# Kernel tuning notes

Measured on AMD Instinct MI355X. Metric: run time of the kernel, lower is better.

Reference implementation:

```python
import jax, jax.numpy as jnp
import numpy as np

# Grid config (from VoxelGrid.from_config defaults / args_to_config)
LOWER = jnp.array([-4.0, -4.0, -1.0], dtype=jnp.float32)
UPPER = jnp.array([4.0, 4.0, 1.0], dtype=jnp.float32)
RESOLUTION = 25.0
SIZE = (200, 200, 50)  # ceil((upper - lower) * resolution)
N_POINTS = 8388608


def setup_inputs() -> dict:
    key = jax.random.key(0)
    k1, k2 = jax.random.split(key)
    # query points uniform over (slightly beyond) the grid extent; points whose
    # fractional index falls outside [0, size-1] are masked to 0 as in the module
    u = jax.random.uniform(k1, (N_POINTS, 3), dtype=jnp.float32)
    x = LOWER + u * (UPPER - LOWER)
    # learned parameter hk.get_parameter('grid', (*size, 1)); randn instead of
    # zeros-init so outputs/grads are nontrivial
    grid = jax.random.normal(k2, (*SIZE, 1), dtype=jnp.float32) * 0.1
    return {"x": x, "grid": grid}


def _trilinear(x, grid):
    size_i = jnp.array(SIZE, dtype=jnp.int32)
    size_f = jnp.array(SIZE, dtype=jnp.float32)
    idx = (x - LOWER) * RESOLUTION                       # [N, 3] fractional index
    valid = jnp.all((idx >= 0.0) & (idx <= size_f - 1.0), axis=-1)  # [N]
    i0 = jnp.clip(jnp.floor(idx).astype(jnp.int32), 0, size_i - 1)  # [N, 3]
    i1 = jnp.minimum(i0 + 1, size_i - 1)                 # [N, 3]
    f = idx - jnp.floor(idx)                             # [N, 3] trilinear fractions
    w = jnp.stack([1.0 - f, f], axis=-1)                 # [N, 3, 2] per-axis weights
    corners = [(i0[:, d], i1[:, d]) for d in range(3)]
    acc = jnp.zeros(x.shape[0], dtype=grid.dtype)
    # 8 fixed corner gathers (structural, not a data-dim loop)
    for a in (0, 1):
        for b in (0, 1):
            for c in (0, 1):
                v = grid[corners[0][a], corners[1][b], corners[2][c], 0]  # [N]
                acc = acc + v * (w[:, 0, a] * w[:, 1, b] * w[:, 2, c])
    sigma = jnp.where(valid, acc, 0.0)
    return sigma


def reference(x, grid):
    sigma = _trilinear(x, grid)
    alpha = jnp.zeros_like(sigma)  # do_alpha=False -> alpha is constant 0
    return (sigma, alpha)
```

## Files before the change

kernel.cpp:

```cpp
#include <hip/hip_runtime.h>
#include <hip/hip_fp16.h>


constexpr int SX = 200, SY = 200, SZ = 50;
constexpr int NVOX = SX * SY * SZ;
constexpr int CX = SX - 1, CY = SY - 1, CZ = SZ - 1;
constexpr int NCELL = CX * CY * CZ;
constexpr int PPT = 4;
constexpr int BLK = 256;
constexpr int PPB = BLK * PPT;


__global__ __launch_bounds__(256) void grid_absmax(
    const float4* __restrict__ g4, unsigned int* __restrict__ scale_u)
{
    int tid = blockIdx.x * 256 + threadIdx.x;
    int stride = gridDim.x * 256;
    unsigned int u = 0;
    for (int i = tid; i < NVOX / 4; i += stride) {
        float4 v = g4[i];
        u = max(u, __float_as_uint(v.x) & 0x7fffffffu);
        u = max(u, __float_as_uint(v.y) & 0x7fffffffu);
        u = max(u, __float_as_uint(v.z) & 0x7fffffffu);
        u = max(u, __float_as_uint(v.w) & 0x7fffffffu);
    }
    #pragma unroll
    for (int off = 32; off > 0; off >>= 1)
        u = max(u, (unsigned int)__shfl_xor((int)u, off, 64));
    __shared__ unsigned int wmax[4];
    int lane = threadIdx.x & 63, wid = threadIdx.x >> 6;
    if (lane == 0) wmax[wid] = u;
    __syncthreads();
    if (threadIdx.x == 0) {
        unsigned int m = max(max(wmax[0], wmax[1]), max(wmax[2], wmax[3]));
        atomicMax(scale_u, m);
    }
}

__global__ __launch_bounds__(256) void build_cells_i8(
    const float* __restrict__ grid, uint2* __restrict__ rec,
    const unsigned int* __restrict__ scale_u)
{
    int i = blockIdx.x * 256 + threadIdx.x;
    if (i >= NCELL) return;
    float absmax = __uint_as_float(*scale_u);
    float inv = (absmax > 0.0f) ? 127.0f / absmax : 0.0f;

    int cz = i % CZ;
    int tmp = i / CZ;
    int cy = tmp % CY;
    int cx = tmp / CY;

    const float* g00 = grid + (cx * SY + cy) * SZ + cz;
    const float* g01 = g00 + SZ;
    const float* g10 = g00 + SY * SZ;
    const float* g11 = g10 + SZ;

    float v[8] = { g00[0], g00[1], g01[0], g01[1],
                   g10[0], g10[1], g11[0], g11[1] };
    unsigned int lo = 0, hi = 0;
    #pragma unroll
    for (int k = 0; k < 4; ++k) {
        int q = (int)rintf(v[k] * inv);
        q = min(max(q, -127), 127);
        lo |= ((unsigned int)(q & 0xff)) << (8 * k);
    }
    #pragma unroll
    for (int k = 0; k < 4; ++k) {
        int q = (int)rintf(v[4 + k] * inv);
        q = min(max(q, -127), 127);
        hi |= ((unsigned int)(q & 0xff)) << (8 * k);
    }
    rec[i] = make_uint2(lo, hi);
}

__device__ __forceinline__ float sb(unsigned int w, int k)
{
    return (float)((int)(w << (24 - 8 * k)) >> 24);
}

__global__ __launch_bounds__(256) void voxel_trilinear_i8(
    const float* __restrict__ x,
    const uint2* __restrict__ rec,
    const unsigned int* __restrict__ scale_u,
    float* __restrict__ out,
    int n)
{
    __shared__ float xs[3 * PPB];
    int tid = threadIdx.x;
    long long base = (long long)blockIdx.x * PPB;
    float s = __uint_as_float(*scale_u) * (1.0f / 127.0f);

    if (base + PPB <= n) {
        const float4* xg = (const float4*)(x + base * 3);
        float4* xl = (float4*)xs;
        #pragma unroll
        for (int j = 0; j < 3; ++j)
            xl[tid + BLK * j] = xg[tid + BLK * j];
    } else {
        for (int j = tid; j < 3 * PPB; j += BLK) {
            long long g = base * 3 + j;
            xs[j] = (g < 3LL * n) ? x[g] : 0.0f;
        }
    }
    __syncthreads();

    int   cell[PPT];
    float ux[PPT], uy[PPT], uz[PPT];
    bool  valid[PPT];

    #pragma unroll
    for (int k = 0; k < PPT; ++k) {
        int p = tid + BLK * k;
        float ix = (xs[3 * p + 0] + 4.0f) * 25.0f;
        float iy = (xs[3 * p + 1] + 4.0f) * 25.0f;
        float iz = (xs[3 * p + 2] + 1.0f) * 25.0f;
        valid[k] = (ix >= 0.0f) & (ix <= (float)(SX - 1)) &
                   (iy >= 0.0f) & (iy <= (float)(SY - 1)) &
                   (iz >= 0.0f) & (iz <= (float)(SZ - 1));
        int cx = min(max((int)floorf(ix), 0), SX - 2);
        int cy = min(max((int)floorf(iy), 0), SY - 2);
        int cz = min(max((int)floorf(iz), 0), SZ - 2);
        ux[k] = ix - (float)cx;
        uy[k] = iy - (float)cy;
        uz[k] = iz - (float)cz;
        cell[k] = (cx * CY + cy) * CZ + cz;
    }

    uint2 pk[PPT];
    #pragma unroll
    for (int k = 0; k < PPT; ++k)
        pk[k] = rec[cell[k]];

    #pragma unroll
    for (int k = 0; k < PPT; ++k) {
        unsigned int lo = pk[k].x, hi = pk[k].y;
        float vz = 1.0f - uz[k], vy = 1.0f - uy[k], vx = 1.0f - ux[k];
        float c00 = sb(lo, 0) * vz + sb(lo, 1) * uz[k];
        float c01 = sb(lo, 2) * vz + sb(lo, 3) * uz[k];
        float c10 = sb(hi, 0) * vz + sb(hi, 1) * uz[k];
        float c11 = sb(hi, 2) * vz + sb(hi, 3) * uz[k];
        float c0 = c00 * vy + c01 * uy[k];
        float c1 = c10 * vy + c11 * uy[k];
        float acc = (c0 * vx + c1 * ux[k]) * s;

        long long i = base + tid + BLK * k;
        if (i < n) {
            out[i] = valid[k] ? acc : 0.0f;
            out[n + i] = 0.0f;
        }
    }
}

__global__ __launch_bounds__(256) void convert_grid_fp16(
    const float* __restrict__ grid, __half* __restrict__ t)
{
    int i = blockIdx.x * 256 + threadIdx.x;
    if (i < NVOX) t[i] = __float2half(grid[i]);
}

__device__ __forceinline__ float2 ldpair(const __half* __restrict__ t, int idx)
{
    __half2 h;
    __builtin_memcpy(&h, t + idx, sizeof(__half2));
    return __half22float2(h);
}

__global__ __launch_bounds__(256) void voxel_trilinear_pair(
    const float* __restrict__ x, const __half* __restrict__ t,
    float* __restrict__ out, int n)
{
    int i = blockIdx.x * 256 + threadIdx.x;
    if (i >= n) return;
    float ix = (x[3 * i + 0] + 4.0f) * 25.0f;
    float iy = (x[3 * i + 1] + 4.0f) * 25.0f;
    float iz = (x[3 * i + 2] + 1.0f) * 25.0f;
    bool valid = (ix >= 0.0f) & (ix <= (float)(SX - 1)) &
                 (iy >= 0.0f) & (iy <= (float)(SY - 1)) &
                 (iz >= 0.0f) & (iz <= (float)(SZ - 1));
    float fx = floorf(ix), fy = floorf(iy), fz = floorf(iz);
    int ax = min(max((int)fx, 0), SX - 1);
    int ay = min(max((int)fy, 0), SY - 1);
    int bx = min(ax + 1, SX - 1);
    int by = min(ay + 1, SY - 1);
    int zc = min(max((int)fz, 0), SZ - 2);
    float u = iz - (float)zc, su = 1.0f - u;
    float tx = ix - fx, ty = iy - fy;
    float sx = 1.0f - tx, sy = 1.0f - ty;
    int r00 = (ax * SY + ay) * SZ + zc;
    int r01 = (ax * SY + by) * SZ + zc;
    int r10 = (bx * SY + ay) * SZ + zc;
    int r11 = (bx * SY + by) * SZ + zc;
    float2 p00 = ldpair(t, r00), p01 = ldpair(t, r01);
    float2 p10 = ldpair(t, r10), p11 = ldpair(t, r11);
    float c00 = p00.x * su + p00.y * u;
    float c01 = p01.x * su + p01.y * u;
    float c10 = p10.x * su + p10.y * u;
    float c11 = p11.x * su + p11.y * u;
    float c0 = c00 * sy + c01 * ty;
    float c1 = c10 * sy + c11 * ty;
    out[i] = valid ? (c0 * sx + c1 * tx) : 0.0f;
    out[n + i] = 0.0f;
}

extern "C" void kernel_launch(void* const* d_in, const int* in_sizes, int n_in,
                              void* d_out, int out_size, void* d_ws, size_t ws_size,
                              hipStream_t stream) {
    const float* x = (const float*)d_in[0];
    const float* grid = (const float*)d_in[1];
    float* out = (float*)d_out;
    int n = in_sizes[0] / 3;

    size_t rec_bytes = (size_t)NCELL * sizeof(uint2);
    if (ws_size >= rec_bytes + 4) {
        uint2* rec = (uint2*)d_ws;
        unsigned int* scale_u = (unsigned int*)((char*)d_ws + rec_bytes);
        hipMemsetAsync(scale_u, 0, 4, stream);
        grid_absmax<<<512, 256, 0, stream>>>((const float4*)grid, scale_u);
        build_cells_i8<<<(NCELL + 255) / 256, 256, 0, stream>>>(grid, rec, scale_u);
        int blocks = (n + PPB - 1) / PPB;
        voxel_trilinear_i8<<<blocks, BLK, 0, stream>>>(x, rec, scale_u, out, n);
    } else if (ws_size >= (size_t)NVOX * sizeof(__half)) {
        __half* t = (__half*)d_ws;
        convert_grid_fp16<<<(NVOX + 255) / 256, 256, 0, stream>>>(grid, t);
        voxel_trilinear_pair<<<(n + 255) / 256, 256, 0, stream>>>(x, t, out, n);
    }
}
```

Baseline: 272.6 us.

## Replace int8 8-corner cell records with 2-byte z-pair table and nontemporal IO

Swaps the 8-byte per-cell int8 record (about 15.6 MB) for a 2-byte z-pair table (about 3.9 MB), so each point now does four 2-byte gathers instead of one 8-byte gather. The table is small enough to stay in cache, while the per-point gather count rises. The atomic absmax plus memset is replaced by per-block partial maxima that are reduced inside the build kernel. Input loads and output stores now use nontemporal hints to keep the streamed data from pushing the table out of cache.

```diff
diff --git a/kernel.cpp b/kernel.cpp
--- a/kernel.cpp
+++ b/kernel.cpp
@@ -1,18 +1,21 @@
 #include <hip/hip_runtime.h>
-#include <hip/hip_fp16.h>
-
+
+
+typedef float vfloat4 __attribute__((ext_vector_type(4)));
 
 constexpr int SX = 200, SY = 200, SZ = 50;
 constexpr int NVOX = SX * SY * SZ;
-constexpr int CX = SX - 1, CY = SY - 1, CZ = SZ - 1;
-constexpr int NCELL = CX * CY * CZ;
+constexpr int CZ = SZ - 1;
+constexpr int NXY = SX * SY;
+constexpr int NREC = NXY * CZ;
 constexpr int PPT = 4;
 constexpr int BLK = 256;
 constexpr int PPB = BLK * PPT;
-
-
-__global__ __launch_bounds__(256) void grid_absmax(
-    const float4* __restrict__ g4, unsigned int* __restrict__ scale_u)
+constexpr int NPART = 512;
+
+
+__global__ __launch_bounds__(256) void grid_absmax_part(
+    const float4* __restrict__ g4, unsigned int* __restrict__ part)
 {
     int tid = blockIdx.x * 256 + threadIdx.x;
     int stride = gridDim.x * 256;
@@ -31,72 +34,70 @@
     int lane = threadIdx.x & 63, wid = threadIdx.x >> 6;
     if (lane == 0) wmax[wid] = u;
     __syncthreads();
+    if (threadIdx.x == 0)
+        part[blockIdx.x] = max(max(wmax[0], wmax[1]), max(wmax[2], wmax[3]));
+}
+
+__global__ __launch_bounds__(256) void build_pairs_i8(
+    const float* __restrict__ grid, unsigned short* __restrict__ tp,
+    const unsigned int* __restrict__ part, float* __restrict__ scale_f)
+{
+    __shared__ unsigned int wmax[4];
+    __shared__ float s_inv;
+    unsigned int u = max(part[threadIdx.x], part[threadIdx.x + 256]);
+    #pragma unroll
+    for (int off = 32; off > 0; off >>= 1)
+        u = max(u, (unsigned int)__shfl_xor((int)u, off, 64));
+    int lane = threadIdx.x & 63, wid = threadIdx.x >> 6;
+    if (lane == 0) wmax[wid] = u;
+    __syncthreads();
     if (threadIdx.x == 0) {
         unsigned int m = max(max(wmax[0], wmax[1]), max(wmax[2], wmax[3]));
-        atomicMax(scale_u, m);
-    }
-}
-
-__global__ __launch_bounds__(256) void build_cells_i8(
-    const float* __restrict__ grid, uint2* __restrict__ rec,
-    const unsigned int* __restrict__ scale_u)
-{
+        float absmax = __uint_as_float(m);
+        s_inv = (absmax > 0.0f) ? 127.0f / absmax : 0.0f;
+        if (blockIdx.x == 0) *scale_f = absmax * (1.0f / 127.0f);
+    }
+    __syncthreads();
+    float inv = s_inv;
+
     int i = blockIdx.x * 256 + threadIdx.x;
-    if (i >= NCELL) return;
-    float absmax = __uint_as_float(*scale_u);
-    float inv = (absmax > 0.0f) ? 127.0f / absmax : 0.0f;
-
-    int cz = i % CZ;
-    int tmp = i / CZ;
-    int cy = tmp % CY;
-    int cx = tmp / CY;
-
-    const float* g00 = grid + (cx * SY + cy) * SZ + cz;
-    const float* g01 = g00 + SZ;
-    const float* g10 = g00 + SY * SZ;
-    const float* g11 = g10 + SZ;
-
-    float v[8] = { g00[0], g00[1], g01[0], g01[1],
-                   g10[0], g10[1], g11[0], g11[1] };
-    unsigned int lo = 0, hi = 0;
-    #pragma unroll
-    for (int k = 0; k < 4; ++k) {
-        int q = (int)rintf(v[k] * inv);
-        q = min(max(q, -127), 127);
-        lo |= ((unsigned int)(q & 0xff)) << (8 * k);
-    }
-    #pragma unroll
-    for (int k = 0; k < 4; ++k) {
-        int q = (int)rintf(v[4 + k] * inv);
-        q = min(max(q, -127), 127);
-        hi |= ((unsigned int)(q & 0xff)) << (8 * k);
-    }
-    rec[i] = make_uint2(lo, hi);
-}
-
-__device__ __forceinline__ float sb(unsigned int w, int k)
-{
-    return (float)((int)(w << (24 - 8 * k)) >> 24);
-}
-
-__global__ __launch_bounds__(256) void voxel_trilinear_i8(
+    if (i >= NREC) return;
+    int z = i % CZ;
+    int xy = i / CZ;
+    const float* g = grid + xy * SZ + z;
+    float a = g[0], b = g[1];
+    int qa = min(max((int)rintf(a * inv), -127), 127);
+    int qb = min(max((int)rintf(b * inv), -127), 127);
+    tp[i] = (unsigned short)((qa & 0xff) | ((qb & 0xff) << 8));
+}
+
+__device__ __forceinline__ float lob(unsigned int w)
+{
+    return (float)((int)(w << 24) >> 24);
+}
+__device__ __forceinline__ float hib(unsigned int w)
+{
+    return (float)((int)(w << 16) >> 24);
+}
+
+__global__ __launch_bounds__(256) void voxel_trilinear_zp(
     const float* __restrict__ x,
-    const uint2* __restrict__ rec,
-    const unsigned int* __restrict__ scale_u,
+    const unsigned short* __restrict__ tp,
+    const float* __restrict__ scale_f,
     float* __restrict__ out,
     int n)
 {
     __shared__ float xs[3 * PPB];
     int tid = threadIdx.x;
     long long base = (long long)blockIdx.x * PPB;
-    float s = __uint_as_float(*scale_u) * (1.0f / 127.0f);
+    float s = *scale_f;
 
     if (base + PPB <= n) {
-        const float4* xg = (const float4*)(x + base * 3);
-        float4* xl = (float4*)xs;
+        const vfloat4* xg = (const vfloat4*)(x + base * 3);
+        vfloat4* xl = (vfloat4*)xs;
         #pragma unroll
         for (int j = 0; j < 3; ++j)
-            xl[tid + BLK * j] = xg[tid + BLK * j];
+            xl[tid + BLK * j] = __builtin_nontemporal_load(&xg[tid + BLK * j]);
     } else {
         for (int j = tid; j < 3 * PPB; j += BLK) {
             long long g = base * 3 + j;
@@ -105,8 +106,8 @@
     }
     __syncthreads();
 
-    int   cell[PPT];
     float ux[PPT], uy[PPT], uz[PPT];
+    int   i00[PPT];
     bool  valid[PPT];
 
     #pragma unroll
@@ -124,50 +125,41 @@
         ux[k] = ix - (float)cx;
         uy[k] = iy - (float)cy;
         uz[k] = iz - (float)cz;
-        cell[k] = (cx * CY + cy) * CZ + cz;
-    }
-
-    uint2 pk[PPT];
-    #pragma unroll
-    for (int k = 0; k < PPT; ++k)
-        pk[k] = rec[cell[k]];
-
+        i00[k] = (cx * SY + cy) * CZ + cz;
+    }
+
+    unsigned int p00[PPT], p01[PPT], p10[PPT], p11[PPT];
     #pragma unroll
     for (int k = 0; k < PPT; ++k) {
-        unsigned int lo = pk[k].x, hi = pk[k].y;
-        float vz = 1.0f - uz[k], vy = 1.0f - uy[k], vx = 1.0f - ux[k];
-        float c00 = sb(lo, 0) * vz + sb(lo, 1) * uz[k];
-        float c01 = sb(lo, 2) * vz + sb(lo, 3) * uz[k];
-        float c10 = sb(hi, 0) * vz + sb(hi, 1) * uz[k];
-        float c11 = sb(hi, 2) * vz + sb(hi, 3) * uz[k];
+        int b = i00[k];
+        p00[k] = tp[b];
+        p01[k] = tp[b + CZ];
+        p10[k] = tp[b + SY * CZ];
+        p11[k] = tp[b + SY * CZ + CZ];
+    }
+
+    #pragma unroll
+    for (int k = 0; k < PPT; ++k) {
+        float w1 = uz[k], w0 = 1.0f - w1;
+        float c00 = lob(p00[k]) * w0 + hib(p00[k]) * w1;
+        float c01 = lob(p01[k]) * w0 + hib(p01[k]) * w1;
+        float c10 = lob(p10[k]) * w0 + hib(p10[k]) * w1;
+        float c11 = lob(p11[k]) * w0 + hib(p11[k]) * w1;
+        float vy = 1.0f - uy[k], vx = 1.0f - ux[k];
         float c0 = c00 * vy + c01 * uy[k];
         float c1 = c10 * vy + c11 * uy[k];
         float acc = (c0 * vx + c1 * ux[k]) * s;
 
         long long i = base + tid + BLK * k;
         if (i < n) {
-            out[i] = valid[k] ? acc : 0.0f;
-            out[n + i] = 0.0f;
+            __builtin_nontemporal_store(valid[k] ? acc : 0.0f, &out[i]);
+            __builtin_nontemporal_store(0.0f, &out[n + i]);
         }
     }
 }
 
-__global__ __launch_bounds__(256) void convert_grid_fp16(
-    const float* __restrict__ grid, __half* __restrict__ t)
-{
-    int i = blockIdx.x * 256 + threadIdx.x;
-    if (i < NVOX) t[i] = __float2half(grid[i]);
-}
-
-__device__ __forceinline__ float2 ldpair(const __half* __restrict__ t, int idx)
-{
-    __half2 h;
-    __builtin_memcpy(&h, t + idx, sizeof(__half2));
-    return __half22float2(h);
-}
-
-__global__ __launch_bounds__(256) void voxel_trilinear_pair(
-    const float* __restrict__ x, const __half* __restrict__ t,
+__global__ __launch_bounds__(256) void voxel_trilinear_direct(
+    const float* __restrict__ x, const float* __restrict__ grid,
     float* __restrict__ out, int n)
 {
     int i = blockIdx.x * 256 + threadIdx.x;
@@ -178,28 +170,23 @@
     bool valid = (ix >= 0.0f) & (ix <= (float)(SX - 1)) &
                  (iy >= 0.0f) & (iy <= (float)(SY - 1)) &
                  (iz >= 0.0f) & (iz <= (float)(SZ - 1));
-    float fx = floorf(ix), fy = floorf(iy), fz = floorf(iz);
-    int ax = min(max((int)fx, 0), SX - 1);
-    int ay = min(max((int)fy, 0), SY - 1);
-    int bx = min(ax + 1, SX - 1);
-    int by = min(ay + 1, SY - 1);
-    int zc = min(max((int)fz, 0), SZ - 2);
-    float u = iz - (float)zc, su = 1.0f - u;
-    float tx = ix - fx, ty = iy - fy;
-    float sx = 1.0f - tx, sy = 1.0f - ty;
-    int r00 = (ax * SY + ay) * SZ + zc;
-    int r01 = (ax * SY + by) * SZ + zc;
-    int r10 = (bx * SY + ay) * SZ + zc;
-    int r11 = (bx * SY + by) * SZ + zc;
-    float2 p00 = ldpair(t, r00), p01 = ldpair(t, r01);
-    float2 p10 = ldpair(t, r10), p11 = ldpair(t, r11);
-    float c00 = p00.x * su + p00.y * u;
-    float c01 = p01.x * su + p01.y * u;
-    float c10 = p10.x * su + p10.y * u;
-    float c11 = p11.x * su + p11.y * u;
-    float c0 = c00 * sy + c01 * ty;
-    float c1 = c10 * sy + c11 * ty;
-    out[i] = valid ? (c0 * sx + c1 * tx) : 0.0f;
+    int cx = min(max((int)floorf(ix), 0), SX - 2);
+    int cy = min(max((int)floorf(iy), 0), SY - 2);
+    int cz = min(max((int)floorf(iz), 0), SZ - 2);
+    float tx = ix - (float)cx, ty = iy - (float)cy, tz = iz - (float)cz;
+    const float* g = grid + (cx * SY + cy) * SZ + cz;
+    float v000 = g[0], v001 = g[1];
+    float v010 = g[SZ], v011 = g[SZ + 1];
+    float v100 = g[SY * SZ], v101 = g[SY * SZ + 1];
+    float v110 = g[SY * SZ + SZ], v111 = g[SY * SZ + SZ + 1];
+    float sz_ = 1.0f - tz, sy_ = 1.0f - ty, sx_ = 1.0f - tx;
+    float c00 = v000 * sz_ + v001 * tz;
+    float c01 = v010 * sz_ + v011 * tz;
+    float c10 = v100 * sz_ + v101 * tz;
+    float c11 = v110 * sz_ + v111 * tz;
+    float c0 = c00 * sy_ + c01 * ty;
+    float c1 = c10 * sy_ + c11 * ty;
+    out[i] = valid ? (c0 * sx_ + c1 * tx) : 0.0f;
     out[n + i] = 0.0f;
 }
 
@@ -211,18 +198,16 @@
     float* out = (float*)d_out;
     int n = in_sizes[0] / 3;
 
-    size_t rec_bytes = (size_t)NCELL * sizeof(uint2);
-    if (ws_size >= rec_bytes + 4) {
-        uint2* rec = (uint2*)d_ws;
-        unsigned int* scale_u = (unsigned int*)((char*)d_ws + rec_bytes);
-        hipMemsetAsync(scale_u, 0, 4, stream);
-        grid_absmax<<<512, 256, 0, stream>>>((const float4*)grid, scale_u);
-        build_cells_i8<<<(NCELL + 255) / 256, 256, 0, stream>>>(grid, rec, scale_u);
+    size_t need = 4096 + (size_t)NREC * sizeof(unsigned short);
+    if (ws_size >= need) {
+        unsigned int* part = (unsigned int*)d_ws;
+        float* scale_f = (float*)((char*)d_ws + 2048);
+        unsigned short* tp = (unsigned short*)((char*)d_ws + 4096);
+        grid_absmax_part<<<NPART, 256, 0, stream>>>((const float4*)grid, part);
+        build_pairs_i8<<<(NREC + 255) / 256, 256, 0, stream>>>(grid, tp, part, scale_f);
         int blocks = (n + PPB - 1) / PPB;
-        voxel_trilinear_i8<<<blocks, BLK, 0, stream>>>(x, rec, scale_u, out, n);
-    } else if (ws_size >= (size_t)NVOX * sizeof(__half)) {
-        __half* t = (__half*)d_ws;
-        convert_grid_fp16<<<(NVOX + 255) / 256, 256, 0, stream>>>(grid, t);
-        voxel_trilinear_pair<<<(n + 255) / 256, 256, 0, stream>>>(x, t, out, n);
-    }
-}
+        voxel_trilinear_zp<<<blocks, BLK, 0, stream>>>(x, tp, scale_f, out, n);
+    } else {
+        voxel_trilinear_direct<<<(n + 255) / 256, 256, 0, stream>>>(x, grid, out, n);
+    }
+}
```

Result: slower. 278.5 us (+2.2%).
